# Performance work log

Hardware: AMD Instinct MI355X
Metric: run time of the kernel (lower is better)

Reference implementation:

```python
import jax, jax.numpy as jnp
import numpy as np

N_NODES = 100000
N_EDGES = 3200000
N_GRAPHS = 32
D_IN = 128
D_HID = 128
N_CLASSES = 10


def setup_inputs() -> dict:
    key = jax.random.key(0)
    ks = jax.random.split(key, 16)
    h = jax.random.normal(ks[0], (N_NODES, D_IN), dtype=jnp.float32)
    src = jax.random.randint(ks[1], (N_EDGES,), 0, N_NODES, dtype=jnp.int32)
    dst = jax.random.randint(ks[2], (N_EDGES,), 0, N_NODES, dtype=jnp.int32)
    graph_ids = jnp.sort(jax.random.randint(ks[3], (N_NODES,), 0, N_GRAPHS, dtype=jnp.int32))
    def lin(k, fi, fo):
        s = 1.0 / np.sqrt(fi)
        kw, kb = jax.random.split(k)
        W = jax.random.uniform(kw, (fi, fo), minval=-s, maxval=s, dtype=jnp.float32)
        b = jax.random.uniform(kb, (fo,), minval=-s, maxval=s, dtype=jnp.float32)
        return W, b
    W1, b1 = lin(ks[4], D_IN, D_HID)
    W2, b2 = lin(ks[5], D_HID, D_HID)
    W3, b3 = lin(ks[6], D_HID, D_HID)
    W4, b4 = lin(ks[7], D_HID, D_HID)
    Wc1, bc1 = lin(ks[8], D_HID, D_HID)
    Wc2, bc2 = lin(ks[9], D_HID, N_CLASSES)
    return {"h": h, "src": src, "dst": dst, "graph_ids": graph_ids,
            "W1": W1, "b1": b1, "W2": W2, "b2": b2, "W3": W3, "b3": b3,
            "W4": W4, "b4": b4, "Wc1": Wc1, "bc1": bc1, "Wc2": Wc2, "bc2": bc2}


def _graph_conv(h, src, dst, inv_sqrt_out, inv_sqrt_in, W, b):
    # DGL GraphConv, norm='both': D_dst^{-1/2} A D_src^{-1/2} h W + b
    m = (h * inv_sqrt_out[:, None])[src]            # [E, D] gathered messages
    agg = jax.ops.segment_sum(m, dst, num_segments=h.shape[0])  # [N, D]
    return (agg * inv_sqrt_in[:, None]) @ W + b


def reference(h, src, dst, graph_ids, W1, b1, W2, b2, W3, b3, W4, b4, Wc1, bc1, Wc2, bc2):
    n = h.shape[0]
    ones_e = jnp.ones(src.shape[0], dtype=jnp.float32)
    out_deg = jnp.clip(jax.ops.segment_sum(ones_e, src, num_segments=n), 1.0)
    in_deg = jnp.clip(jax.ops.segment_sum(ones_e, dst, num_segments=n), 1.0)
    inv_sqrt_out = jax.lax.rsqrt(out_deg)
    inv_sqrt_in = jax.lax.rsqrt(in_deg)

    x = jax.nn.relu(_graph_conv(h, src, dst, inv_sqrt_out, inv_sqrt_in, W1, b1))
    x = jax.nn.relu(_graph_conv(x, src, dst, inv_sqrt_out, inv_sqrt_in, W2, b2))
    x = jax.nn.relu(_graph_conv(x, src, dst, inv_sqrt_out, inv_sqrt_in, W3, b3))
    x = jax.nn.relu(_graph_conv(x, src, dst, inv_sqrt_out, inv_sqrt_in, W4, b4))

    # dgl.mean_nodes over batched graphs
    sums = jax.ops.segment_sum(x, graph_ids, num_segments=N_GRAPHS)     # [G, D]
    counts = jax.ops.segment_sum(jnp.ones(n, dtype=jnp.float32), graph_ids, num_segments=N_GRAPHS)
    hg = sums / jnp.clip(counts, 1.0)[:, None]

    out = jax.nn.relu(hg @ Wc1 + bc1)
    out = out @ Wc2 + bc2
    return out
```

## Files before the change

kernel.cpp:

```cpp
#include <hip/hip_runtime.h>

#define D 128
#define NG 32
#define NC 10

typedef unsigned short ushort_t;
typedef __attribute__((ext_vector_type(8))) short short8v;
typedef __attribute__((ext_vector_type(4))) float float4v;
typedef __attribute__((ext_vector_type(2))) float float2v;

__device__ __forceinline__ ushort_t f2bf(float x) {
  union { float f; unsigned u; } v; v.f = x;
  unsigned r = (v.u + 0x7FFF + ((v.u >> 16) & 1)) >> 16;
  return (ushort_t)r;
}
__device__ __forceinline__ float bf2f(ushort_t b) {
  union { unsigned u; float f; } v; v.u = ((unsigned)b) << 16;
  return v.f;
}

__global__ void degree_kernel(const int* __restrict__ src, const int* __restrict__ dst,
                              int* __restrict__ cout_, int* __restrict__ cursor,
                              int* __restrict__ rank, int E) {
  int i = blockIdx.x * 256 + threadIdx.x;
  int e0 = i * 4;
  if (e0 + 4 <= E) {
    int4 s = *(const int4*)(src + e0);
    int4 d_ = *(const int4*)(dst + e0);
    int r0 = atomicAdd(&cursor[d_.x], 1);
    int r1 = atomicAdd(&cursor[d_.y], 1);
    int r2 = atomicAdd(&cursor[d_.z], 1);
    int r3 = atomicAdd(&cursor[d_.w], 1);
    atomicAdd(&cout_[s.x], 1);
    atomicAdd(&cout_[s.y], 1);
    atomicAdd(&cout_[s.z], 1);
    atomicAdd(&cout_[s.w], 1);
    *(int4*)(rank + e0) = make_int4(r0, r1, r2, r3);
  } else {
    for (int e = e0; e < E; ++e) {
      rank[e] = atomicAdd(&cursor[dst[e]], 1);
      atomicAdd(&cout_[src[e]], 1);
    }
  }
}

__global__ void scan1_kernel(const int* __restrict__ cnt, int* __restrict__ bsum, int n) {
  __shared__ int sdata[256];
  int base = blockIdx.x * 1024 + threadIdx.x * 4;
  int s = 0;
#pragma unroll
  for (int j = 0; j < 4; ++j) {
    int idx = base + j;
    if (idx < n) s += cnt[idx];
  }
  sdata[threadIdx.x] = s;
  __syncthreads();
  for (int off = 128; off > 0; off >>= 1) {
    if (threadIdx.x < off) sdata[threadIdx.x] += sdata[threadIdx.x + off];
    __syncthreads();
  }
  if (threadIdx.x == 0) bsum[blockIdx.x] = sdata[0];
}

__global__ void scan2_kernel(int* __restrict__ bsum, int nb) {
  if (blockIdx.x == 0 && threadIdx.x == 0) {
    int acc = 0;
    for (int i = 0; i < nb; ++i) { int v = bsum[i]; bsum[i] = acc; acc += v; }
  }
}

__global__ void scan3_kernel(const int* __restrict__ cnt, const int* __restrict__ bsum,
                             int* __restrict__ rowptr, int n, int e_total) {
  __shared__ int ss[256];
  int t = threadIdx.x;
  int idx0 = blockIdx.x * 1024 + t * 4;
  int v[4]; int ts = 0;
#pragma unroll
  for (int j = 0; j < 4; ++j) {
    v[j] = (idx0 + j < n) ? cnt[idx0 + j] : 0;
    ts += v[j];
  }
  ss[t] = ts;
  __syncthreads();
  for (int off = 1; off < 256; off <<= 1) {
    int add = 0;
    if (t >= off) add = ss[t - off];
    __syncthreads();
    if (t >= off) ss[t] += add;
    __syncthreads();
  }
  int excl = ss[t] - ts + bsum[blockIdx.x];
#pragma unroll
  for (int j = 0; j < 4; ++j) {
    int idx = idx0 + j;
    if (idx < n) rowptr[idx] = excl;
    excl += v[j];
  }
  if (blockIdx.x == 0 && t == 0) rowptr[n] = e_total;
}

__global__ void passB_kernel(const int* __restrict__ src, const int* __restrict__ dst,
                             const int* __restrict__ rank, const int* __restrict__ rowptr,
                             int* __restrict__ csrc, int E) {
  int i = blockIdx.x * 256 + threadIdx.x;
  int e0 = i * 4;
  if (e0 + 4 <= E) {
    int4 s = *(const int4*)(src + e0);
    int4 d_ = *(const int4*)(dst + e0);
    int4 r = *(const int4*)(rank + e0);
    csrc[rowptr[d_.x] + r.x] = s.x;
    csrc[rowptr[d_.y] + r.y] = s.y;
    csrc[rowptr[d_.z] + r.z] = s.z;
    csrc[rowptr[d_.w] + r.w] = s.w;
  } else {
    for (int e = e0; e < E; ++e)
      csrc[rowptr[dst[e]] + rank[e]] = src[e];
  }
}

__global__ void cvt_h_kernel(const float* __restrict__ h, ushort_t* __restrict__ hb, long total) {
  long i4 = ((long)blockIdx.x * 256 + threadIdx.x) * 4;
  if (i4 + 4 <= total) {
    float4 v = *(const float4*)(h + i4);
    ushort_t o[4] = { f2bf(v.x), f2bf(v.y), f2bf(v.z), f2bf(v.w) };
    *(uint2*)(hb + i4) = *(const uint2*)o;
  } else {
    for (long i = i4; i < total; ++i) hb[i] = f2bf(h[i]);
  }
}

__global__ void cvt_w_kernel(const float* __restrict__ W1, const float* __restrict__ W2,
                             const float* __restrict__ W3, const float* __restrict__ W4,
                             ushort_t* __restrict__ Wt) {
  const float* Ws[4] = { W1, W2, W3, W4 };
  const float* W = Ws[blockIdx.x];
  ushort_t* o = Wt + (size_t)blockIdx.x * D * D;
  for (int idx = threadIdx.x; idx < D * D; idx += 256) {
    int c = idx >> 7, k = idx & 127;
    o[c * D + k] = f2bf(W[k * D + c]);
  }
}

__global__ __launch_bounds__(256) void gemm_mfma_kernel(const ushort_t* __restrict__ A,
    const ushort_t* __restrict__ Wt, const int* __restrict__ cout_,
    unsigned char* __restrict__ X, int n) {
  int wave = threadIdx.x >> 6;
  int lane = threadIdx.x & 63;
  int g = lane >> 4;
  int lr = lane & 15;
  int rowbase = blockIdx.x * 64 + wave * 16;
  int arow = rowbase + lr;
  int arow_c = arow < n ? arow : (n - 1);
  const ushort_t* Ap = A + (size_t)arow_c * D + g * 8;

  short8v afrag[4];
#pragma unroll
  for (int ks = 0; ks < 4; ++ks)
    afrag[ks] = *(const short8v*)(Ap + ks * 32);

  float4v acc[8];
#pragma unroll
  for (int ct = 0; ct < 8; ++ct)
#pragma unroll
    for (int r = 0; r < 4; ++r) acc[ct][r] = 0.f;

#pragma unroll
  for (int ct = 0; ct < 8; ++ct) {
    const ushort_t* bp = Wt + (size_t)(ct * 16 + lr) * D + g * 8;
#pragma unroll
    for (int ks = 0; ks < 4; ++ks) {
      short8v bfrag = *(const short8v*)(bp + ks * 32);
      acc[ct] = __builtin_amdgcn_mfma_f32_16x16x32_bf16(afrag[ks], bfrag, acc[ct], 0, 0, 0);
    }
  }

  float scv[4];
  bool rok[4];
#pragma unroll
  for (int r = 0; r < 4; ++r) {
    int grow = rowbase + g * 4 + r;
    rok[r] = grow < n;
    int gc = rok[r] ? grow : (n - 1);
    scv[r] = rsqrtf(fmaxf((float)cout_[gc], 1.f));
  }
#pragma unroll
  for (int ct = 0; ct < 8; ++ct) {
#pragma unroll
    for (int r = 0; r < 4; ++r) {
      int grow = rowbase + g * 4 + r;
      if (rok[r]) {
        int p = __builtin_amdgcn_cvt_pk_fp8_f32(acc[ct][r] * scv[r], 0.f, 0, false);
        X[(size_t)grow * D + ct * 16 + lr] = (unsigned char)(p & 0xff);
      }
    }
  }
}

__global__ __launch_bounds__(256) void agg_relu_kernel(const unsigned char* __restrict__ x,
    const int* __restrict__ rowptr, const int* __restrict__ csrc,
    const int* __restrict__ cin_, const float* __restrict__ bias,
    ushort_t* __restrict__ y, int n) {
  int node = blockIdx.x * 4 + (threadIdx.x >> 6);
  if (node >= n) return;
  int lane = threadIdx.x & 63;
  int beg = rowptr[node], end = rowptr[node + 1];
  float ax = 0.f, ay = 0.f;
  const unsigned char* xp = x + lane * 2;
  int e = beg;
  for (; e + 8 <= end; e += 8) {
    int s[8];
#pragma unroll
    for (int j = 0; j < 8; ++j) s[j] = csrc[e + j];
    ushort_t u[8];
#pragma unroll
    for (int j = 0; j < 8; ++j) u[j] = *(const ushort_t*)(xp + (size_t)s[j] * D);
#pragma unroll
    for (int j = 0; j < 8; ++j) {
      float2v f = __builtin_amdgcn_cvt_pk_f32_fp8((unsigned)u[j], false);
      ax += f[0]; ay += f[1];
    }
  }
  if (e + 4 <= end) {
    int s[4];
#pragma unroll
    for (int j = 0; j < 4; ++j) s[j] = csrc[e + j];
    ushort_t u[4];
#pragma unroll
    for (int j = 0; j < 4; ++j) u[j] = *(const ushort_t*)(xp + (size_t)s[j] * D);
#pragma unroll
    for (int j = 0; j < 4; ++j) {
      float2v f = __builtin_amdgcn_cvt_pk_f32_fp8((unsigned)u[j], false);
      ax += f[0]; ay += f[1];
    }
    e += 4;
  }
  for (; e < end; ++e) {
    int s = csrc[e];
    ushort_t u = *(const ushort_t*)(xp + (size_t)s * D);
    float2v f = __builtin_amdgcn_cvt_pk_f32_fp8((unsigned)u, false);
    ax += f[0]; ay += f[1];
  }
  float wi = rsqrtf(fmaxf((float)cin_[node], 1.f));
  float2 bb = *(const float2*)(bias + lane * 2);
  ushort_t o[2] = { f2bf(fmaxf(ax * wi + bb.x, 0.f)), f2bf(fmaxf(ay * wi + bb.y, 0.f)) };
  *(unsigned*)(y + (size_t)node * D + lane * 2) = *(const unsigned*)o;
}

__device__ int lower_bound_gid(const int* gid, int n, int g) {
  int lo = 0, hi = n;
  while (lo < hi) { int mid = (lo + hi) >> 1; if (gid[mid] < g) lo = mid + 1; else hi = mid; }
  return lo;
}

__global__ void pool_kernel(const ushort_t* __restrict__ x, const int* __restrict__ gid,
                            float* __restrict__ sums, int* __restrict__ counts, int n) {
  int g = blockIdx.x >> 3, part = blockIdx.x & 7;
  __shared__ int s_lo, s_hi;
  if (threadIdx.x == 0) {
    s_lo = lower_bound_gid(gid, n, g);
    s_hi = lower_bound_gid(gid, n, g + 1);
    if (part == 0) counts[g] = s_hi - s_lo;
  }
  __syncthreads();
  int lo = s_lo, hi = s_hi;
  int cnt = hi - lo;
  int per = (cnt + 7) >> 3;
  int a = lo + part * per;
  int bnd = min(a + per, hi);
  int t = threadIdx.x;
  float acc = 0.f;
  for (int i = a; i < bnd; ++i) acc += bf2f(x[(size_t)i * D + t]);
  atomicAdd(&sums[g * D + t], acc);
}

__global__ __launch_bounds__(128) void classifier_kernel(const float* __restrict__ sums,
    const int* __restrict__ counts, const float* __restrict__ Wc1, const float* __restrict__ bc1,
    const float* __restrict__ Wc2, const float* __restrict__ bc2, float* __restrict__ out) {
  __shared__ float hg[NG][D];
  __shared__ float hid[NG][D];
  int t = threadIdx.x;
#pragma unroll
  for (int g = 0; g < NG; ++g)
    hg[g][t] = sums[g * D + t] / fmaxf((float)counts[g], 1.f);
  __syncthreads();
  float acc[NG];
#pragma unroll
  for (int g = 0; g < NG; ++g) acc[g] = bc1[t];
  for (int k = 0; k < D; ++k) {
    float w = Wc1[k * D + t];
#pragma unroll
    for (int g = 0; g < NG; ++g) acc[g] += hg[g][k] * w;
  }
#pragma unroll
  for (int g = 0; g < NG; ++g) hid[g][t] = fmaxf(acc[g], 0.f);
  __syncthreads();
  for (int idx = t; idx < NG * NC; idx += 128) {
    int g = idx / NC, c = idx % NC;
    float a = bc2[c];
    for (int j = 0; j < D; ++j) a += hid[g][j] * Wc2[j * NC + c];
    out[idx] = a;
  }
}

extern "C" void kernel_launch(void* const* d_in, const int* in_sizes, int n_in,
                              void* d_out, int out_size, void* d_ws, size_t ws_size,
                              hipStream_t stream) {
  const float* h   = (const float*)d_in[0];
  const int* src   = (const int*)d_in[1];
  const int* dst   = (const int*)d_in[2];
  const int* gid   = (const int*)d_in[3];
  const float* W1  = (const float*)d_in[4];
  const float* b1  = (const float*)d_in[5];
  const float* W2  = (const float*)d_in[6];
  const float* b2  = (const float*)d_in[7];
  const float* W3  = (const float*)d_in[8];
  const float* b3  = (const float*)d_in[9];
  const float* W4  = (const float*)d_in[10];
  const float* b4  = (const float*)d_in[11];
  const float* Wc1 = (const float*)d_in[12];
  const float* bc1 = (const float*)d_in[13];
  const float* Wc2 = (const float*)d_in[14];
  const float* bc2 = (const float*)d_in[15];
  float* out = (float*)d_out;

  const int N = in_sizes[3];
  const int E = in_sizes[1];

  char* ws = (char*)d_ws;
  size_t off = 0;
  auto alloc = [&](size_t bytes) -> char* {
    char* p = ws + off;
    off = (off + bytes + 255) & ~(size_t)255;
    return p;
  };

  int* cnts     = (int*)alloc((size_t)2 * N * 4);
  int* cout_    = cnts;
  int* cursor   = cnts + N;
  int* rowptr   = (int*)alloc((size_t)(N + 1) * 4);
  int* bsum     = (int*)alloc(1024);
  int* csrc     = (int*)alloc((size_t)E * 4);
  ushort_t* Wt  = (ushort_t*)alloc((size_t)4 * D * D * 2);
  unsigned char* Xb = (unsigned char*)alloc((size_t)N * D);
  ushort_t* Yb  = (ushort_t*)alloc((size_t)N * D * 2);
  float* sums   = (float*)alloc((size_t)(NG * D + NG) * 4);
  int* counts   = (int*)(sums + NG * D);
  int* rank     = (int*)Yb;
  ushort_t* Hb  = Yb;

  hipMemsetAsync(cnts, 0, (size_t)2 * N * 4, stream);
  hipMemsetAsync(sums, 0, (size_t)(NG * D + NG) * 4, stream);

  int gE4 = (E / 4 + 255) / 256 + 1;
  int nb  = (N + 1023) / 1024;
  int gAgg  = (N + 3) / 4;
  int gGemm = (N + 63) / 64;
  long totalH = (long)N * D;
  int gCvt = (int)((totalH / 4 + 255) / 256) + 1;

  degree_kernel<<<gE4, 256, 0, stream>>>(src, dst, cout_, cursor, rank, E);
  scan1_kernel<<<nb, 256, 0, stream>>>(cursor, bsum, N);
  scan2_kernel<<<1, 64, 0, stream>>>(bsum, nb);
  scan3_kernel<<<nb, 256, 0, stream>>>(cursor, bsum, rowptr, N, E);
  passB_kernel<<<gE4, 256, 0, stream>>>(src, dst, rank, rowptr, csrc, E);

  cvt_w_kernel<<<4, 256, 0, stream>>>(W1, W2, W3, W4, Wt);
  cvt_h_kernel<<<gCvt, 256, 0, stream>>>(h, Hb, totalH);

  gemm_mfma_kernel<<<gGemm, 256, 0, stream>>>(Hb, Wt, cout_, Xb, N);
  agg_relu_kernel<<<gAgg, 256, 0, stream>>>(Xb, rowptr, csrc, cursor, b1, Yb, N);
  gemm_mfma_kernel<<<gGemm, 256, 0, stream>>>(Yb, Wt + (size_t)1 * D * D, cout_, Xb, N);
  agg_relu_kernel<<<gAgg, 256, 0, stream>>>(Xb, rowptr, csrc, cursor, b2, Yb, N);
  gemm_mfma_kernel<<<gGemm, 256, 0, stream>>>(Yb, Wt + (size_t)2 * D * D, cout_, Xb, N);
  agg_relu_kernel<<<gAgg, 256, 0, stream>>>(Xb, rowptr, csrc, cursor, b3, Yb, N);
  gemm_mfma_kernel<<<gGemm, 256, 0, stream>>>(Yb, Wt + (size_t)3 * D * D, cout_, Xb, N);
  agg_relu_kernel<<<gAgg, 256, 0, stream>>>(Xb, rowptr, csrc, cursor, b4, Yb, N);

  pool_kernel<<<NG * 8, 128, 0, stream>>>(Yb, gid, sums, counts, N);
  classifier_kernel<<<1, 128, 0, stream>>>(sums, counts, Wc1, bc1, Wc2, bc2, out);
}
```

Baseline: 955.8 us.

## Replace global out-degree atomics with LDS histogram and widen aggregation loads

Out-degree counting moves out of the ticket kernel into a 32-block LDS histogram. Each block makes 4 passes over all of src, one per 25600-bin window, writes a per-block partial array, and a separate kernel reduces the partials. The aggregation kernel now splits each wavefront into four 16-lane groups that each gather 8 fp8 bytes per edge with a uint2 load, then combines the groups with cross-lane shuffles, so fewer, wider memory transactions cover the same work. Risks: only 32 blocks run the histogram, and each re-reads src four times, which may underuse the GPU. The partial array also adds extra memory traffic.

```diff
diff --git a/kernel.cpp b/kernel.cpp
--- a/kernel.cpp
+++ b/kernel.cpp
@@ -3,6 +3,8 @@
 #define D 128
 #define NG 32
 #define NC 10
+#define HIST_NB 32
+#define HIST_BINS 25600
 
 typedef unsigned short ushort_t;
 typedef __attribute__((ext_vector_type(8))) short short8v;
@@ -19,28 +21,51 @@
   return v.f;
 }
 
-__global__ void degree_kernel(const int* __restrict__ src, const int* __restrict__ dst,
-                              int* __restrict__ cout_, int* __restrict__ cursor,
+__global__ void ticket_kernel(const int* __restrict__ dst, int* __restrict__ cursor,
                               int* __restrict__ rank, int E) {
   int i = blockIdx.x * 256 + threadIdx.x;
   int e0 = i * 4;
   if (e0 + 4 <= E) {
-    int4 s = *(const int4*)(src + e0);
     int4 d_ = *(const int4*)(dst + e0);
     int r0 = atomicAdd(&cursor[d_.x], 1);
     int r1 = atomicAdd(&cursor[d_.y], 1);
     int r2 = atomicAdd(&cursor[d_.z], 1);
     int r3 = atomicAdd(&cursor[d_.w], 1);
-    atomicAdd(&cout_[s.x], 1);
-    atomicAdd(&cout_[s.y], 1);
-    atomicAdd(&cout_[s.z], 1);
-    atomicAdd(&cout_[s.w], 1);
     *(int4*)(rank + e0) = make_int4(r0, r1, r2, r3);
   } else {
-    for (int e = e0; e < E; ++e) {
+    for (int e = e0; e < E; ++e)
       rank[e] = atomicAdd(&cursor[dst[e]], 1);
-      atomicAdd(&cout_[src[e]], 1);
+  }
+}
+
+__global__ __launch_bounds__(256) void hist_kernel(const int* __restrict__ src,
+    int* __restrict__ partial, int E, int n) {
+  __shared__ int lh[HIST_BINS];
+  int b = blockIdx.x;
+  int npass = (n + HIST_BINS - 1) / HIST_BINS;
+  for (int p = 0; p < npass; ++p) {
+    int base = p * HIST_BINS;
+    int bins = min(HIST_BINS, n - base);
+    for (int j = threadIdx.x; j < bins; j += 256) lh[j] = 0;
+    __syncthreads();
+    for (int e = b * 256 + threadIdx.x; e < E; e += HIST_NB * 256) {
+      int s = src[e] - base;
+      if ((unsigned)s < (unsigned)bins) atomicAdd(&lh[s], 1);
     }
+    __syncthreads();
+    int* out = partial + (size_t)b * n + base;
+    for (int j = threadIdx.x; j < bins; j += 256) out[j] = lh[j];
+    __syncthreads();
+  }
+}
+
+__global__ void histreduce_kernel(const int* __restrict__ partial, int* __restrict__ cout_, int n) {
+  int i = blockIdx.x * 256 + threadIdx.x;
+  if (i < n) {
+    int s = 0;
+#pragma unroll
+    for (int b = 0; b < HIST_NB; ++b) s += partial[(size_t)b * n + i];
+    cout_[i] = s;
   }
 }
 
@@ -203,47 +228,62 @@
   int node = blockIdx.x * 4 + (threadIdx.x >> 6);
   if (node >= n) return;
   int lane = threadIdx.x & 63;
+  int q = lane >> 4;
+  int lr = lane & 15;
   int beg = rowptr[node], end = rowptr[node + 1];
-  float ax = 0.f, ay = 0.f;
-  const unsigned char* xp = x + lane * 2;
+  float acc[8];
+#pragma unroll
+  for (int j = 0; j < 8; ++j) acc[j] = 0.f;
+
+  const unsigned char* xp = x + lr * 8;
   int e = beg;
   for (; e + 8 <= end; e += 8) {
-    int s[8];
-#pragma unroll
-    for (int j = 0; j < 8; ++j) s[j] = csrc[e + j];
-    ushort_t u[8];
-#pragma unroll
-    for (int j = 0; j < 8; ++j) u[j] = *(const ushort_t*)(xp + (size_t)s[j] * D);
-#pragma unroll
-    for (int j = 0; j < 8; ++j) {
-      float2v f = __builtin_amdgcn_cvt_pk_f32_fp8((unsigned)u[j], false);
-      ax += f[0]; ay += f[1];
+    int e0 = csrc[e + q];
+    int e1 = csrc[e + 4 + q];
+    uint2 u0 = *(const uint2*)(xp + (size_t)e0 * D);
+    uint2 u1 = *(const uint2*)(xp + (size_t)e1 * D);
+    float2v f;
+    f = __builtin_amdgcn_cvt_pk_f32_fp8(u0.x, false); acc[0] += f[0]; acc[1] += f[1];
+    f = __builtin_amdgcn_cvt_pk_f32_fp8(u0.x, true);  acc[2] += f[0]; acc[3] += f[1];
+    f = __builtin_amdgcn_cvt_pk_f32_fp8(u0.y, false); acc[4] += f[0]; acc[5] += f[1];
+    f = __builtin_amdgcn_cvt_pk_f32_fp8(u0.y, true);  acc[6] += f[0]; acc[7] += f[1];
+    f = __builtin_amdgcn_cvt_pk_f32_fp8(u1.x, false); acc[0] += f[0]; acc[1] += f[1];
+    f = __builtin_amdgcn_cvt_pk_f32_fp8(u1.x, true);  acc[2] += f[0]; acc[3] += f[1];
+    f = __builtin_amdgcn_cvt_pk_f32_fp8(u1.y, false); acc[4] += f[0]; acc[5] += f[1];
+    f = __builtin_amdgcn_cvt_pk_f32_fp8(u1.y, true);  acc[6] += f[0]; acc[7] += f[1];
+  }
+  for (; e < end; e += 4) {
+    int ee = e + q;
+    if (ee < end) {
+      int s = csrc[ee];
+      uint2 u = *(const uint2*)(xp + (size_t)s * D);
+      float2v f;
+      f = __builtin_amdgcn_cvt_pk_f32_fp8(u.x, false); acc[0] += f[0]; acc[1] += f[1];
+      f = __builtin_amdgcn_cvt_pk_f32_fp8(u.x, true);  acc[2] += f[0]; acc[3] += f[1];
+      f = __builtin_amdgcn_cvt_pk_f32_fp8(u.y, false); acc[4] += f[0]; acc[5] += f[1];
+      f = __builtin_amdgcn_cvt_pk_f32_fp8(u.y, true);  acc[6] += f[0]; acc[7] += f[1];
     }
   }
-  if (e + 4 <= end) {
-    int s[4];
-#pragma unroll
-    for (int j = 0; j < 4; ++j) s[j] = csrc[e + j];
-    ushort_t u[4];
-#pragma unroll
-    for (int j = 0; j < 4; ++j) u[j] = *(const ushort_t*)(xp + (size_t)s[j] * D);
-#pragma unroll
-    for (int j = 0; j < 4; ++j) {
-      float2v f = __builtin_amdgcn_cvt_pk_f32_fp8((unsigned)u[j], false);
-      ax += f[0]; ay += f[1];
-    }
-    e += 4;
-  }
-  for (; e < end; ++e) {
-    int s = csrc[e];
-    ushort_t u = *(const ushort_t*)(xp + (size_t)s * D);
-    float2v f = __builtin_amdgcn_cvt_pk_f32_fp8((unsigned)u, false);
-    ax += f[0]; ay += f[1];
-  }
-  float wi = rsqrtf(fmaxf((float)cin_[node], 1.f));
-  float2 bb = *(const float2*)(bias + lane * 2);
-  ushort_t o[2] = { f2bf(fmaxf(ax * wi + bb.x, 0.f)), f2bf(fmaxf(ay * wi + bb.y, 0.f)) };
-  *(unsigned*)(y + (size_t)node * D + lane * 2) = *(const unsigned*)o;
+#pragma unroll
+  for (int j = 0; j < 8; ++j) {
+    acc[j] += __shfl_xor(acc[j], 16, 64);
+    acc[j] += __shfl_xor(acc[j], 32, 64);
+  }
+  if (q == 0) {
+    float wi = rsqrtf(fmaxf((float)cin_[node], 1.f));
+    float4 b0 = *(const float4*)(bias + lr * 8);
+    float4 b1 = *(const float4*)(bias + lr * 8 + 4);
+    ushort_t o[8];
+    o[0] = f2bf(fmaxf(acc[0] * wi + b0.x, 0.f));
+    o[1] = f2bf(fmaxf(acc[1] * wi + b0.y, 0.f));
+    o[2] = f2bf(fmaxf(acc[2] * wi + b0.z, 0.f));
+    o[3] = f2bf(fmaxf(acc[3] * wi + b0.w, 0.f));
+    o[4] = f2bf(fmaxf(acc[4] * wi + b1.x, 0.f));
+    o[5] = f2bf(fmaxf(acc[5] * wi + b1.y, 0.f));
+    o[6] = f2bf(fmaxf(acc[6] * wi + b1.z, 0.f));
+    o[7] = f2bf(fmaxf(acc[7] * wi + b1.w, 0.f));
+    *(uint4*)(y + (size_t)node * D + lr * 8) = *(const uint4*)o;
+  }
 }
 
 __device__ int lower_bound_gid(const int* gid, int n, int g) {
@@ -341,24 +381,30 @@
   int* bsum     = (int*)alloc(1024);
   int* csrc     = (int*)alloc((size_t)E * 4);
   ushort_t* Wt  = (ushort_t*)alloc((size_t)4 * D * D * 2);
-  unsigned char* Xb = (unsigned char*)alloc((size_t)N * D);
+  size_t xb_bytes = (size_t)N * D;
+  size_t hist_bytes = (size_t)HIST_NB * N * 4;
+  unsigned char* Xb = (unsigned char*)alloc(xb_bytes > hist_bytes ? xb_bytes : hist_bytes);
   ushort_t* Yb  = (ushort_t*)alloc((size_t)N * D * 2);
   float* sums   = (float*)alloc((size_t)(NG * D + NG) * 4);
   int* counts   = (int*)(sums + NG * D);
   int* rank     = (int*)Yb;
   ushort_t* Hb  = Yb;
-
-  hipMemsetAsync(cnts, 0, (size_t)2 * N * 4, stream);
+  int* partial  = (int*)Xb;
+
+  hipMemsetAsync(cursor, 0, (size_t)N * 4, stream);
   hipMemsetAsync(sums, 0, (size_t)(NG * D + NG) * 4, stream);
 
   int gE4 = (E / 4 + 255) / 256 + 1;
+  int gN  = (N + 255) / 256;
   int nb  = (N + 1023) / 1024;
   int gAgg  = (N + 3) / 4;
   int gGemm = (N + 63) / 64;
   long totalH = (long)N * D;
   int gCvt = (int)((totalH / 4 + 255) / 256) + 1;
 
-  degree_kernel<<<gE4, 256, 0, stream>>>(src, dst, cout_, cursor, rank, E);
+  ticket_kernel<<<gE4, 256, 0, stream>>>(dst, cursor, rank, E);
+  hist_kernel<<<HIST_NB, 256, 0, stream>>>(src, partial, E, N);
+  histreduce_kernel<<<gN, 256, 0, stream>>>(partial, cout_, N);
   scan1_kernel<<<nb, 256, 0, stream>>>(cursor, bsum, N);
   scan2_kernel<<<1, 64, 0, stream>>>(bsum, nb);
   scan3_kernel<<<nb, 256, 0, stream>>>(cursor, bsum, rowptr, N, E);
```

New measurement: 1.083 ms. 13.3% more time.

## Tile fp8 features into 32-column slabs and split aggregation across column quarters

Applied to the files above, without the earlier changes.

The GEMM now writes its fp8 output as four column slabs of 32 bytes per node instead of 128-byte rows. The aggregation kernel gets a second grid dimension over these quarters. Within each wave, 8 edge slots each gather 4 bytes per lane and are combined with cross-lane shuffles. This gives each slab a smaller working set for better cache locality and more edges in flight per wave, at the cost of reloading indices four times and extra shuffle reductions. The serial single-thread block-sum scan is also replaced with a parallel 1024-thread shared-memory scan.

```diff
diff --git a/kernel.cpp b/kernel.cpp
--- a/kernel.cpp
+++ b/kernel.cpp
@@ -63,10 +63,18 @@
 }
 
 __global__ void scan2_kernel(int* __restrict__ bsum, int nb) {
-  if (blockIdx.x == 0 && threadIdx.x == 0) {
-    int acc = 0;
-    for (int i = 0; i < nb; ++i) { int v = bsum[i]; bsum[i] = acc; acc += v; }
-  }
+  __shared__ int s[1024];
+  int t = threadIdx.x;
+  int v = (t < nb) ? bsum[t] : 0;
+  s[t] = v;
+  __syncthreads();
+  for (int off = 1; off < 1024; off <<= 1) {
+    int add = (t >= off) ? s[t - off] : 0;
+    __syncthreads();
+    s[t] += add;
+    __syncthreads();
+  }
+  if (t < nb) bsum[t] = s[t] - v;
 }
 
 __global__ void scan3_kernel(const int* __restrict__ cnt, const int* __restrict__ bsum,
@@ -185,16 +193,23 @@
   }
 #pragma unroll
   for (int ct = 0; ct < 8; ++ct) {
+    int qq = ct >> 1;
+    int c32 = (ct & 1) * 16 + lr;
 #pragma unroll
     for (int r = 0; r < 4; ++r) {
       int grow = rowbase + g * 4 + r;
       if (rok[r]) {
         int p = __builtin_amdgcn_cvt_pk_fp8_f32(acc[ct][r] * scv[r], 0.f, 0, false);
-        X[(size_t)grow * D + ct * 16 + lr] = (unsigned char)(p & 0xff);
+        X[((size_t)qq * n + grow) * 32 + c32] = (unsigned char)(p & 0xff);
       }
     }
   }
 }
+
+#define ACC4(u)                                                                  \
+  { float2v f;                                                                   \
+    f = __builtin_amdgcn_cvt_pk_f32_fp8((u), false); acc[0] += f[0]; acc[1] += f[1]; \
+    f = __builtin_amdgcn_cvt_pk_f32_fp8((u), true);  acc[2] += f[0]; acc[3] += f[1]; }
 
 __global__ __launch_bounds__(256) void agg_relu_kernel(const unsigned char* __restrict__ x,
     const int* __restrict__ rowptr, const int* __restrict__ csrc,
@@ -202,48 +217,63 @@
     ushort_t* __restrict__ y, int n) {
   int node = blockIdx.x * 4 + (threadIdx.x >> 6);
   if (node >= n) return;
+  int qq = blockIdx.y;
   int lane = threadIdx.x & 63;
+  int slot = lane >> 3;
+  int lr = lane & 7;
   int beg = rowptr[node], end = rowptr[node + 1];
-  float ax = 0.f, ay = 0.f;
-  const unsigned char* xp = x + lane * 2;
+  float acc[4];
+#pragma unroll
+  for (int j = 0; j < 4; ++j) acc[j] = 0.f;
+
+  const unsigned char* xq = x + (size_t)qq * n * 32 + lr * 4;
   int e = beg;
+
+  int pro = (beg + 3) & ~3;
+  if (pro > beg) {
+    int ee = beg + slot;
+    if (ee < end && ee < pro) {
+      int s = csrc[ee];
+      unsigned u = *(const unsigned*)(xq + (size_t)s * 32);
+      ACC4(u);
+    }
+    e = pro < end ? pro : end;
+  }
+  for (; e + 32 <= end; e += 32) {
+    int4 s4 = *(const int4*)(csrc + e + slot * 4);
+    unsigned u0 = *(const unsigned*)(xq + (size_t)s4.x * 32);
+    unsigned u1 = *(const unsigned*)(xq + (size_t)s4.y * 32);
+    unsigned u2 = *(const unsigned*)(xq + (size_t)s4.z * 32);
+    unsigned u3 = *(const unsigned*)(xq + (size_t)s4.w * 32);
+    ACC4(u0); ACC4(u1); ACC4(u2); ACC4(u3);
+  }
   for (; e + 8 <= end; e += 8) {
-    int s[8];
-#pragma unroll
-    for (int j = 0; j < 8; ++j) s[j] = csrc[e + j];
-    ushort_t u[8];
-#pragma unroll
-    for (int j = 0; j < 8; ++j) u[j] = *(const ushort_t*)(xp + (size_t)s[j] * D);
-#pragma unroll
-    for (int j = 0; j < 8; ++j) {
-      float2v f = __builtin_amdgcn_cvt_pk_f32_fp8((unsigned)u[j], false);
-      ax += f[0]; ay += f[1];
-    }
-  }
-  if (e + 4 <= end) {
-    int s[4];
-#pragma unroll
-    for (int j = 0; j < 4; ++j) s[j] = csrc[e + j];
-    ushort_t u[4];
-#pragma unroll
-    for (int j = 0; j < 4; ++j) u[j] = *(const ushort_t*)(xp + (size_t)s[j] * D);
-#pragma unroll
-    for (int j = 0; j < 4; ++j) {
-      float2v f = __builtin_amdgcn_cvt_pk_f32_fp8((unsigned)u[j], false);
-      ax += f[0]; ay += f[1];
-    }
-    e += 4;
-  }
-  for (; e < end; ++e) {
-    int s = csrc[e];
-    ushort_t u = *(const ushort_t*)(xp + (size_t)s * D);
-    float2v f = __builtin_amdgcn_cvt_pk_f32_fp8((unsigned)u, false);
-    ax += f[0]; ay += f[1];
-  }
-  float wi = rsqrtf(fmaxf((float)cin_[node], 1.f));
-  float2 bb = *(const float2*)(bias + lane * 2);
-  ushort_t o[2] = { f2bf(fmaxf(ax * wi + bb.x, 0.f)), f2bf(fmaxf(ay * wi + bb.y, 0.f)) };
-  *(unsigned*)(y + (size_t)node * D + lane * 2) = *(const unsigned*)o;
+    int s = csrc[e + slot];
+    unsigned u = *(const unsigned*)(xq + (size_t)s * 32);
+    ACC4(u);
+  }
+  if (e + slot < end) {
+    int s = csrc[e + slot];
+    unsigned u = *(const unsigned*)(xq + (size_t)s * 32);
+    ACC4(u);
+  }
+
+#pragma unroll
+  for (int j = 0; j < 4; ++j) {
+    acc[j] += __shfl_xor(acc[j], 8, 64);
+    acc[j] += __shfl_xor(acc[j], 16, 64);
+    acc[j] += __shfl_xor(acc[j], 32, 64);
+  }
+  if (slot == 0) {
+    float wi = rsqrtf(fmaxf((float)cin_[node], 1.f));
+    float4 bb = *(const float4*)(bias + qq * 32 + lr * 4);
+    ushort_t o[4];
+    o[0] = f2bf(fmaxf(acc[0] * wi + bb.x, 0.f));
+    o[1] = f2bf(fmaxf(acc[1] * wi + bb.y, 0.f));
+    o[2] = f2bf(fmaxf(acc[2] * wi + bb.z, 0.f));
+    o[3] = f2bf(fmaxf(acc[3] * wi + bb.w, 0.f));
+    *(uint2*)(y + (size_t)node * D + qq * 32 + lr * 4) = *(const uint2*)o;
+  }
 }
 
 __device__ int lower_bound_gid(const int* gid, int n, int g) {
@@ -338,7 +368,7 @@
   int* cout_    = cnts;
   int* cursor   = cnts + N;
   int* rowptr   = (int*)alloc((size_t)(N + 1) * 4);
-  int* bsum     = (int*)alloc(1024);
+  int* bsum     = (int*)alloc(4096);
   int* csrc     = (int*)alloc((size_t)E * 4);
   ushort_t* Wt  = (ushort_t*)alloc((size_t)4 * D * D * 2);
   unsigned char* Xb = (unsigned char*)alloc((size_t)N * D);
@@ -357,10 +387,11 @@
   int gGemm = (N + 63) / 64;
   long totalH = (long)N * D;
   int gCvt = (int)((totalH / 4 + 255) / 256) + 1;
+  dim3 aggGrid(gAgg, 4);
 
   degree_kernel<<<gE4, 256, 0, stream>>>(src, dst, cout_, cursor, rank, E);
   scan1_kernel<<<nb, 256, 0, stream>>>(cursor, bsum, N);
-  scan2_kernel<<<1, 64, 0, stream>>>(bsum, nb);
+  scan2_kernel<<<1, 1024, 0, stream>>>(bsum, nb);
   scan3_kernel<<<nb, 256, 0, stream>>>(cursor, bsum, rowptr, N, E);
   passB_kernel<<<gE4, 256, 0, stream>>>(src, dst, rank, rowptr, csrc, E);
 
@@ -368,13 +399,13 @@
   cvt_h_kernel<<<gCvt, 256, 0, stream>>>(h, Hb, totalH);
 
   gemm_mfma_kernel<<<gGemm, 256, 0, stream>>>(Hb, Wt, cout_, Xb, N);
-  agg_relu_kernel<<<gAgg, 256, 0, stream>>>(Xb, rowptr, csrc, cursor, b1, Yb, N);
+  agg_relu_kernel<<<aggGrid, 256, 0, stream>>>(Xb, rowptr, csrc, cursor, b1, Yb, N);
   gemm_mfma_kernel<<<gGemm, 256, 0, stream>>>(Yb, Wt + (size_t)1 * D * D, cout_, Xb, N);
-  agg_relu_kernel<<<gAgg, 256, 0, stream>>>(Xb, rowptr, csrc, cursor, b2, Yb, N);
+  agg_relu_kernel<<<aggGrid, 256, 0, stream>>>(Xb, rowptr, csrc, cursor, b2, Yb, N);
   gemm_mfma_kernel<<<gGemm, 256, 0, stream>>>(Yb, Wt + (size_t)2 * D * D, cout_, Xb, N);
-  agg_relu_kernel<<<gAgg, 256, 0, stream>>>(Xb, rowptr, csrc, cursor, b3, Yb, N);
+  agg_relu_kernel<<<aggGrid, 256, 0, stream>>>(Xb, rowptr, csrc, cursor, b3, Yb, N);
   gemm_mfma_kernel<<<gGemm, 256, 0, stream>>>(Yb, Wt + (size_t)3 * D * D, cout_, Xb, N);
-  agg_relu_kernel<<<gAgg, 256, 0, stream>>>(Xb, rowptr, csrc, cursor, b4, Yb, N);
+  agg_relu_kernel<<<aggGrid, 256, 0, stream>>>(Xb, rowptr, csrc, cursor, b4, Yb, N);
 
   pool_kernel<<<NG * 8, 128, 0, stream>>>(Yb, gid, sums, counts, N);
   classifier_kernel<<<1, 128, 0, stream>>>(sums, counts, Wc1, bc1, Wc2, bc2, out);
```

Measured after the change: 1.371 ms. 1.43x slower.
